# Kernel tuning notes

Hardware: AMD Instinct MI355X
Metric: run time of the kernel (lower is better)

The kernel has to match this reference:

```python
import jax, jax.numpy as jnp
import numpy as np

BLOCK_SIZE = 32
BLOCK_COUNTS = 4
NEG = -1e9
SEQ_LENS = np.array([512, 384, 448, 256], dtype=np.int64)


def setup_inputs():
    key = jax.random.key(0)
    ks = jax.random.split(key, 5)
    T = int(SEQ_LENS.sum()); H = 4; D = 64
    offs = np.concatenate([[0], np.cumsum(SEQ_LENS)]).astype(np.int64)
    return {
        "q": jax.random.normal(ks[0], (T, H, D), jnp.float32),
        "k": jax.random.normal(ks[1], (T, H, D), jnp.float32),
        "v": jax.random.normal(ks[2], (T, H, D), jnp.float32),
        "g_cmp": jax.random.uniform(ks[3], (T, H), jnp.float32),
        "g_slc": jax.random.uniform(ks[4], (T, H), jnp.float32),
        "x_offsets": jnp.asarray(offs),
    }


def _silu(x):
    return x * jax.nn.sigmoid(x)


def _forward(q, k, v, g_cmp, g_slc, offs):
    bs = BLOCK_SIZE
    B = len(offs) - 1
    seq_lens = offs[1:] - offs[:-1]              # np [B]
    T, H, D = q.shape
    max_n = int(seq_lens.max())
    nb = (max_n + bs - 1) // bs                  # max compressed blocks
    L = nb * bs                                  # padded length (multiple of bs)
    batch_ids = np.repeat(np.arange(B), seq_lens)
    local_ids = np.arange(T) - offs[:-1][batch_ids]

    def pad(x):  # jagged [T, ...] -> padded [B, L, ...]
        return jnp.zeros((B, L) + x.shape[1:], x.dtype).at[batch_ids, local_ids].set(x)

    pq, pk, pv = pad(q), pad(k), pad(v)
    # block-pooled (mean) compressed K/V; partial blocks also divided by bs, as in torch
    k_cmp = pk.reshape(B, nb, bs, H, D).sum(axis=2) / bs   # [B, nb, H, D]
    v_cmp = pv.reshape(B, nb, bs, H, D).sum(axis=2) / bs

    scale = D ** -0.5
    pos = np.arange(max_n)                       # local query positions
    qblk = pos // bs
    blk = np.arange(nb)
    causal = qblk[:, None] >= blk[None, :]       # [max_n, nb]
    seq_valid = pos[None, :] < seq_lens[:, None]  # [B, max_n]
    cmp_lens = (seq_lens + bs - 1) // bs
    blk_valid = blk[None, :] < cmp_lens[:, None]  # [B, nb]

    pq_m = pq[:, :max_n]                          # [B, max_n, H, D]
    scores = jnp.einsum('bqhd,bkhd->bhqk', pq_m, k_cmp) * scale  # [B,H,max_n,nb]

    # --- compressed branch: mask to -1e9, SiLU, zero masked (matches cmp kernel) ---
    m_full = (jnp.asarray(causal)[None, None]
              & jnp.asarray(seq_valid)[:, None, :, None]
              & jnp.asarray(blk_valid)[:, None, None, :])
    m_zero = jnp.asarray(causal)[None, None] & jnp.asarray(blk_valid)[:, None, None, :]
    p_cmp = jnp.where(m_zero, _silu(jnp.where(m_full, scores, NEG)), 0.0)
    o_cmp_pad = jnp.einsum('bhqk,bkhd->bqhd', p_cmp, v_cmp)
    o_cmp_pad = o_cmp_pad * pad(g_cmp)[:, :max_n, :, None]
    o_cmp = o_cmp_pad[batch_ids, local_ids]       # back to jagged [T,H,D]

    # --- per-token top-S block selection on causally masked compressed scores ---
    sel_scores = jnp.where(jnp.asarray(causal)[None, None], scores, -jnp.inf)
    S = min(BLOCK_COUNTS, nb)
    _, topk = jax.lax.top_k(sel_scores, S)        # [B,H,max_n,S] block ids

    # --- selected branch: gather raw K/V from the chosen blocks ---
    r = np.arange(bs)
    tpos = topk[..., None] * bs + r               # [B,H,max_n,S,bs] local key pos < L
    pk_h = pk.transpose(0, 2, 1, 3)               # [B,H,L,D]
    pv_h = pv.transpose(0, 2, 1, 3)
    idx = tpos.reshape(B, H, -1)
    k_sel = jnp.take_along_axis(pk_h, idx[..., None], axis=2).reshape(B, H, max_n, S, bs, D)
    v_sel = jnp.take_along_axis(pv_h, idx[..., None], axis=2).reshape(B, H, max_n, S, bs, D)
    pq_h = pq_m.transpose(0, 2, 1, 3)             # [B,H,max_n,D]
    s_slc = jnp.einsum('bhmd,bhmsrd->bhmsr', pq_h, k_sel) * scale
    within = tpos < jnp.asarray(seq_lens)[:, None, None, None, None]
    caus = tpos <= jnp.asarray(pos)[None, None, :, None, None]
    p_slc = jnp.where(within & caus, _silu(s_slc), 0.0)
    o_slc_pad = jnp.einsum('bhmsr,bhmsrd->bmhd', p_slc, v_sel)
    o_slc_pad = o_slc_pad * pad(g_slc)[:, :max_n, :, None]
    o_slc = o_slc_pad[batch_ids, local_ids]
    return o_cmp, o_slc


def reference(q, k, v, g_cmp, g_slc, x_offsets):
    return _forward(q, k, v, g_cmp, g_slc, np.asarray(x_offsets))
```

## Files before the change

kernel.cpp:

```cpp
#include <hip/hip_runtime.h>
#include <hip/hip_bf16.h>
#include <math.h>

#define HH 4
#define DD 64
#define BS 32
#define SSEL 4
#define STRIDE (HH * DD)

typedef __attribute__((ext_vector_type(8))) short bf16x8;
typedef __attribute__((ext_vector_type(4))) float f32x4;

__device__ __forceinline__ float silu_f(float x) { return x / (1.0f + __expf(-x)); }

__device__ __forceinline__ unsigned int pk2bf(float a, float b) {
    union { __hip_bfloat16 h[2]; unsigned int u; } cu;
    cu.h[0] = __float2bfloat16(a);
    cu.h[1] = __float2bfloat16(b);
    return cu.u;
}

__global__ __launch_bounds__(512, 2) void nsa_all(
        const float* __restrict__ q, const float* __restrict__ k,
        const float* __restrict__ v, const float* __restrict__ gc,
        const float* __restrict__ gs, const int* __restrict__ offs,
        int B, int T, float* __restrict__ out) {
    __shared__ float Qf[32][68];
    __shared__ float Kc[16][68];
    __shared__ float Vc[16][64];
    __shared__ unsigned int Msk[32];
    __shared__ unsigned short Qs[32][64];
    __shared__ __align__(16) char UN[4 * 32 * 68 * 4];

    unsigned int (*Pw)[32][20] = (unsigned int (*)[32][20])UN;
    float        (*Op)[32][68] = (float (*)[32][68])UN;

    int qbh = blockIdx.x;
    int h   = qbh & (HH - 1);
    int qb  = qbh / HH;

    int b = -1, lb = 0, cum = 0, off = 0, n = 0;
    for (int i = 0; i < B; ++i) {
        int o0 = offs[i], o1 = offs[i + 1];
        int nbi = (o1 - o0 + BS - 1) / BS;
        if (qb < cum + nbi) { b = i; lb = qb - cum; off = o0; n = o1 - o0; break; }
        cum += nbi;
    }
    if (b < 0) return;
    int t0  = off + lb * BS;
    int nbl = lb + 1;
    const float scale = 0.125f;
    int tid = threadIdx.x;
    int w = tid >> 6, lane = tid & 63;
    int l15 = lane & 15, g = lane >> 4;

    {
        int row = tid >> 4, dg = tid & 15;
        int trow = min(t0 + row, T - 1);
        float4 a = *(const float4*)(q + (size_t)trow * STRIDE + h * DD + dg * 4);
        a.x *= scale; a.y *= scale; a.z *= scale; a.w *= scale;
        *(float4*)&Qf[row][dg * 4] = a;
        uint2 uu = { pk2bf(a.x, a.y), pk2bf(a.z, a.w) };
        *(uint2*)&Qs[row][(((dg >> 1) ^ (row & 7)) * 8) + (dg & 1) * 4] = uu;
    }

    if (tid < nbl * 32) {
        int j = tid >> 5, rest = tid & 31, kind = rest >> 4, d4 = rest & 15;
        const float* base = (kind ? v : k) + (size_t)(off + j * BS) * STRIDE + h * DD + d4 * 4;
        float4 acc = {0.f, 0.f, 0.f, 0.f};
        #pragma unroll
        for (int r = 0; r < BS; ++r) {
            float4 x = *(const float4*)(base + (size_t)r * STRIDE);
            acc.x += x.x; acc.y += x.y; acc.z += x.z; acc.w += x.w;
        }
        acc.x *= (1.f / BS); acc.y *= (1.f / BS); acc.z *= (1.f / BS); acc.w *= (1.f / BS);
        if (kind) *(float4*)&Vc[j][d4 * 4] = acc;
        else      *(float4*)&Kc[j][d4 * 4] = acc;
    }
    __syncthreads();

    {
        int qq = tid >> 4, j = tid & 15;
        int base16 = lane & 48;
        float s = -INFINITY, p = 0.f;
        if (j < nbl) {
            s = 0.f;
            #pragma unroll
            for (int i = 0; i < 16; ++i) {
                float4 qv = *(float4*)&Qf[qq][i * 4];
                float4 kk = *(float4*)&Kc[j][i * 4];
                s += qv.x * kk.x + qv.y * kk.y + qv.z * kk.z + qv.w * kk.w;
            }
            p = silu_f(s);
        }
        int rank = 0;
        #pragma unroll
        for (int i = 0; i < 16; ++i) {
            float si = __shfl(s, base16 | i, 64);
            rank += (si > s) || (si == s && i < j);
        }
        bool sel = (j < nbl) && (rank < SSEL);
        unsigned long long bal = __ballot(sel);
        if (j == 0) Msk[qq] = (unsigned int)((bal >> base16) & 0xFFFFull);

        float4 o = {0.f, 0.f, 0.f, 0.f};
        for (int blk = 0; blk < nbl; ++blk) {
            float pb = __shfl(p, base16 | blk, 64);
            float4 vv = *(float4*)&Vc[blk][j * 4];
            o.x += pb * vv.x; o.y += pb * vv.y; o.z += pb * vv.z; o.w += pb * vv.w;
        }
        if (lb * BS + qq < n) {
            float gv = gc[(size_t)(t0 + qq) * HH + h];
            o.x *= gv; o.y *= gv; o.z *= gv; o.w *= gv;
            *(float4*)(out + (size_t)(t0 + qq) * STRIDE + h * DD + j * 4) = o;
        }
    }
    __syncthreads();

    unsigned int Msq[2];
    Msq[0] = Msk[l15];
    Msq[1] = Msk[16 + l15];

    f32x4 oacc[4][2];
    #pragma unroll
    for (int dt = 0; dt < 4; ++dt)
        #pragma unroll
        for (int qt = 0; qt < 2; ++qt)
            oacc[dt][qt] = (f32x4){0.f, 0.f, 0.f, 0.f};

    #pragma unroll 1
    for (int kb = w; kb <= lb; kb += 8) {
        const float* kbase = k + (size_t)(off + kb * BS) * STRIDE + h * DD;
        const float* vbase = v + (size_t)(off + kb * BS) * STRIDE + h * DD;

        float tv[4][8];
        #pragma unroll
        for (int dt = 0; dt < 4; ++dt)
            #pragma unroll
            for (int j = 0; j < 8; ++j)
                tv[dt][j] = vbase[(size_t)(g * 8 + j) * STRIDE + dt * 16 + l15];

        float4 kf[2][2][2];
        #pragma unroll
        for (int tt = 0; tt < 2; ++tt)
            #pragma unroll
            for (int ds = 0; ds < 2; ++ds) {
                const float4* p = (const float4*)(kbase + (size_t)(tt * 16 + l15) * STRIDE
                                                  + ds * 32 + g * 8);
                kf[tt][ds][0] = p[0];
                kf[tt][ds][1] = p[1];
            }

        bf16x8 a1[2][2];
        #pragma unroll
        for (int tt = 0; tt < 2; ++tt)
            #pragma unroll
            for (int ds = 0; ds < 2; ++ds) {
                union { unsigned int u[4]; bf16x8 v8; } cu;
                float4 x = kf[tt][ds][0], y = kf[tt][ds][1];
                cu.u[0] = pk2bf(x.x, x.y); cu.u[1] = pk2bf(x.z, x.w);
                cu.u[2] = pk2bf(y.x, y.y); cu.u[3] = pk2bf(y.z, y.w);
                a1[tt][ds] = cu.v8;
            }
        bf16x8 b1[2][2];
        #pragma unroll
        for (int ds = 0; ds < 2; ++ds)
            #pragma unroll
            for (int tt = 0; tt < 2; ++tt)
                b1[tt][ds] = *(bf16x8*)&Qs[tt * 16 + l15][((g + ds * 4) ^ (l15 & 7)) * 8];

        f32x4 s[2][2];
        #pragma unroll
        for (int kt = 0; kt < 2; ++kt)
            #pragma unroll
            for (int qt = 0; qt < 2; ++qt) {
                s[kt][qt] = (f32x4){0.f, 0.f, 0.f, 0.f};
                s[kt][qt] = __builtin_amdgcn_mfma_f32_16x16x32_bf16(a1[kt][0], b1[qt][0], s[kt][qt], 0, 0, 0);
                s[kt][qt] = __builtin_amdgcn_mfma_f32_16x16x32_bf16(a1[kt][1], b1[qt][1], s[kt][qt], 0, 0, 0);
            }

        #pragma unroll
        for (int kt = 0; kt < 2; ++kt)
            #pragma unroll
            for (int qt = 0; qt < 2; ++qt) {
                bool selbit = (Msq[qt] >> kb) & 1u;
                float pv[4];
                #pragma unroll
                for (int r = 0; r < 4; ++r) {
                    int k_l = kt * 16 + g * 4 + r;
                    int q_l = qt * 16 + l15;
                    bool ok = selbit && (kb < lb || k_l <= q_l);
                    pv[r] = ok ? silu_f(s[kt][qt][r]) : 0.f;
                }
                Pw[w][qt * 16 + l15][kt * 8 + g * 2 + 0] = pk2bf(pv[0], pv[1]);
                Pw[w][qt * 16 + l15][kt * 8 + g * 2 + 1] = pk2bf(pv[2], pv[3]);
            }
        bf16x8 b2[2];
        b2[0] = *(bf16x8*)&Pw[w][l15][g * 4];
        b2[1] = *(bf16x8*)&Pw[w][16 + l15][g * 4];

        bf16x8 a2[4];
        #pragma unroll
        for (int dt = 0; dt < 4; ++dt) {
            union { unsigned int u[4]; bf16x8 v8; } cu;
            cu.u[0] = pk2bf(tv[dt][0], tv[dt][1]);
            cu.u[1] = pk2bf(tv[dt][2], tv[dt][3]);
            cu.u[2] = pk2bf(tv[dt][4], tv[dt][5]);
            cu.u[3] = pk2bf(tv[dt][6], tv[dt][7]);
            a2[dt] = cu.v8;
        }

        #pragma unroll
        for (int dt = 0; dt < 4; ++dt)
            #pragma unroll
            for (int qt = 0; qt < 2; ++qt)
                oacc[dt][qt] = __builtin_amdgcn_mfma_f32_16x16x32_bf16(a2[dt], b2[qt], oacc[dt][qt], 0, 0, 0);
    }
    __syncthreads();

    if (w < 4) {
        #pragma unroll
        for (int dt = 0; dt < 4; ++dt)
            #pragma unroll
            for (int qt = 0; qt < 2; ++qt)
                #pragma unroll
                for (int r = 0; r < 4; ++r)
                    Op[w][qt * 16 + l15][dt * 16 + g * 4 + r] = oacc[dt][qt][r];
    }
    __syncthreads();
    if (w >= 4) {
        #pragma unroll
        for (int dt = 0; dt < 4; ++dt)
            #pragma unroll
            for (int qt = 0; qt < 2; ++qt)
                #pragma unroll
                for (int r = 0; r < 4; ++r)
                    Op[w - 4][qt * 16 + l15][dt * 16 + g * 4 + r] += oacc[dt][qt][r];
    }
    __syncthreads();

    {
        int qq = tid >> 4, dg = tid & 15;
        if (lb * BS + qq < n) {
            float gv = gs[(size_t)(t0 + qq) * HH + h];
            float o[4];
            #pragma unroll
            for (int i = 0; i < 4; ++i) {
                int d = dg * 4 + i;
                o[i] = (Op[0][qq][d] + Op[1][qq][d] + Op[2][qq][d] + Op[3][qq][d]) * gv;
            }
            *(float4*)(out + (size_t)T * STRIDE + (size_t)(t0 + qq) * STRIDE + h * DD + dg * 4)
                = (float4){o[0], o[1], o[2], o[3]};
        }
    }
}

extern "C" void kernel_launch(void* const* d_in, const int* in_sizes, int n_in,
                              void* d_out, int out_size, void* d_ws, size_t ws_size,
                              hipStream_t stream) {
    const float* q    = (const float*)d_in[0];
    const float* k    = (const float*)d_in[1];
    const float* v    = (const float*)d_in[2];
    const float* gc   = (const float*)d_in[3];
    const float* gs   = (const float*)d_in[4];
    const int*   offs = (const int*)d_in[5];

    int B = in_sizes[5] - 1;
    int T = out_size / (2 * STRIDE);
    int nbcap  = (T + BS - 1) / BS;
    int nqbcap = nbcap + B;

    nsa_all<<<dim3((unsigned)(nqbcap * HH)), dim3(512), 0, stream>>>(
        q, k, v, gc, gs, offs, B, T, (float*)d_out);
}
```

Measured before the change: 17.61 us.

## Hoist selected-branch K/V loads and QK MFMAs before compressed-branch work

Moves the per-warp loading of raw K/V blocks and the QK^T MFMA to the start of the kernel, before the compressed-branch pooling and top-k phase. This lets global-memory latency and MFMA work overlap with the compressed computation. Q fragments are now built straight from global memory into registers, which removes the swizzled Qs shared array. The loop is unrolled into at most two fixed iterations, so it assumes lb < 16 (sequences up to 512 tokens), and holding both iterations' data in registers raises register pressure.

```diff
diff --git a/kernel.cpp b/kernel.cpp
--- a/kernel.cpp
+++ b/kernel.cpp
@@ -29,7 +29,6 @@
     __shared__ float Kc[16][68];
     __shared__ float Vc[16][64];
     __shared__ unsigned int Msk[32];
-    __shared__ unsigned short Qs[32][64];
     __shared__ __align__(16) char UN[4 * 32 * 68 * 4];
 
     unsigned int (*Pw)[32][20] = (unsigned int (*)[32][20])UN;
@@ -54,14 +53,80 @@
     int w = tid >> 6, lane = tid & 63;
     int l15 = lane & 15, g = lane >> 4;
 
+    bool have0 = (w <= lb);
+    bool have1 = (w + 8 <= lb);
+
+    bf16x8 b1[2][2];
+    #pragma unroll
+    for (int qt = 0; qt < 2; ++qt)
+        #pragma unroll
+        for (int ds = 0; ds < 2; ++ds) {
+            int trow = min(t0 + qt * 16 + l15, T - 1);
+            const float4* p = (const float4*)(q + (size_t)trow * STRIDE + h * DD
+                                              + ds * 32 + g * 8);
+            float4 x = p[0], y = p[1];
+            union { unsigned int u[4]; bf16x8 v8; } cu;
+            cu.u[0] = pk2bf(x.x * scale, x.y * scale);
+            cu.u[1] = pk2bf(x.z * scale, x.w * scale);
+            cu.u[2] = pk2bf(y.x * scale, y.y * scale);
+            cu.u[3] = pk2bf(y.z * scale, y.w * scale);
+            b1[qt][ds] = cu.v8;
+        }
+
+#define LOAD_QKT(KB, A2, SS)                                                            \
+    {                                                                                   \
+        const float* kbase = k + (size_t)(off + (KB) * BS) * STRIDE + h * DD;           \
+        const float* vbase = v + (size_t)(off + (KB) * BS) * STRIDE + h * DD;           \
+        float tv[4][8];                                                                 \
+        _Pragma("unroll")                                                               \
+        for (int dt = 0; dt < 4; ++dt)                                                  \
+            _Pragma("unroll")                                                           \
+            for (int j = 0; j < 8; ++j)                                                 \
+                tv[dt][j] = vbase[(size_t)(g * 8 + j) * STRIDE + dt * 16 + l15];        \
+        bf16x8 a1[2][2];                                                                \
+        _Pragma("unroll")                                                               \
+        for (int tt = 0; tt < 2; ++tt)                                                  \
+            _Pragma("unroll")                                                           \
+            for (int ds = 0; ds < 2; ++ds) {                                            \
+                const float4* p = (const float4*)(kbase + (size_t)(tt * 16 + l15) * STRIDE \
+                                                  + ds * 32 + g * 8);                   \
+                float4 x = p[0], y = p[1];                                              \
+                union { unsigned int u[4]; bf16x8 v8; } cu;                             \
+                cu.u[0] = pk2bf(x.x, x.y); cu.u[1] = pk2bf(x.z, x.w);                   \
+                cu.u[2] = pk2bf(y.x, y.y); cu.u[3] = pk2bf(y.z, y.w);                   \
+                a1[tt][ds] = cu.v8;                                                     \
+            }                                                                           \
+        _Pragma("unroll")                                                               \
+        for (int dt = 0; dt < 4; ++dt) {                                                \
+            union { unsigned int u[4]; bf16x8 v8; } cu;                                 \
+            cu.u[0] = pk2bf(tv[dt][0], tv[dt][1]);                                      \
+            cu.u[1] = pk2bf(tv[dt][2], tv[dt][3]);                                      \
+            cu.u[2] = pk2bf(tv[dt][4], tv[dt][5]);                                      \
+            cu.u[3] = pk2bf(tv[dt][6], tv[dt][7]);                                      \
+            A2[dt] = cu.v8;                                                             \
+        }                                                                               \
+        _Pragma("unroll")                                                               \
+        for (int kt = 0; kt < 2; ++kt)                                                  \
+            _Pragma("unroll")                                                           \
+            for (int qt = 0; qt < 2; ++qt) {                                            \
+                SS[kt][qt] = (f32x4){0.f, 0.f, 0.f, 0.f};                               \
+                SS[kt][qt] = __builtin_amdgcn_mfma_f32_16x16x32_bf16(a1[kt][0], b1[qt][0], SS[kt][qt], 0, 0, 0); \
+                SS[kt][qt] = __builtin_amdgcn_mfma_f32_16x16x32_bf16(a1[kt][1], b1[qt][1], SS[kt][qt], 0, 0, 0); \
+            }                                                                           \
+    }
+
+    bf16x8 a2A[4], a2B[4];
+    f32x4  sA[2][2], sB[2][2];
+    if (have0) LOAD_QKT(w, a2A, sA)
+    if (have1) LOAD_QKT(w + 8, a2B, sB)
+#undef LOAD_QKT
+
     {
         int row = tid >> 4, dg = tid & 15;
         int trow = min(t0 + row, T - 1);
         float4 a = *(const float4*)(q + (size_t)trow * STRIDE + h * DD + dg * 4);
         a.x *= scale; a.y *= scale; a.z *= scale; a.w *= scale;
         *(float4*)&Qf[row][dg * 4] = a;
-        uint2 uu = { pk2bf(a.x, a.y), pk2bf(a.z, a.w) };
-        *(uint2*)&Qs[row][(((dg >> 1) ^ (row & 7)) * 8) + (dg & 1) * 4] = uu;
     }
 
     if (tid < nbl * 32) {
@@ -128,94 +193,38 @@
         for (int qt = 0; qt < 2; ++qt)
             oacc[dt][qt] = (f32x4){0.f, 0.f, 0.f, 0.f};
 
-    #pragma unroll 1
-    for (int kb = w; kb <= lb; kb += 8) {
-        const float* kbase = k + (size_t)(off + kb * BS) * STRIDE + h * DD;
-        const float* vbase = v + (size_t)(off + kb * BS) * STRIDE + h * DD;
-
-        float tv[4][8];
-        #pragma unroll
-        for (int dt = 0; dt < 4; ++dt)
-            #pragma unroll
-            for (int j = 0; j < 8; ++j)
-                tv[dt][j] = vbase[(size_t)(g * 8 + j) * STRIDE + dt * 16 + l15];
-
-        float4 kf[2][2][2];
-        #pragma unroll
-        for (int tt = 0; tt < 2; ++tt)
-            #pragma unroll
-            for (int ds = 0; ds < 2; ++ds) {
-                const float4* p = (const float4*)(kbase + (size_t)(tt * 16 + l15) * STRIDE
-                                                  + ds * 32 + g * 8);
-                kf[tt][ds][0] = p[0];
-                kf[tt][ds][1] = p[1];
-            }
-
-        bf16x8 a1[2][2];
-        #pragma unroll
-        for (int tt = 0; tt < 2; ++tt)
-            #pragma unroll
-            for (int ds = 0; ds < 2; ++ds) {
-                union { unsigned int u[4]; bf16x8 v8; } cu;
-                float4 x = kf[tt][ds][0], y = kf[tt][ds][1];
-                cu.u[0] = pk2bf(x.x, x.y); cu.u[1] = pk2bf(x.z, x.w);
-                cu.u[2] = pk2bf(y.x, y.y); cu.u[3] = pk2bf(y.z, y.w);
-                a1[tt][ds] = cu.v8;
-            }
-        bf16x8 b1[2][2];
-        #pragma unroll
-        for (int ds = 0; ds < 2; ++ds)
-            #pragma unroll
-            for (int tt = 0; tt < 2; ++tt)
-                b1[tt][ds] = *(bf16x8*)&Qs[tt * 16 + l15][((g + ds * 4) ^ (l15 & 7)) * 8];
-
-        f32x4 s[2][2];
-        #pragma unroll
-        for (int kt = 0; kt < 2; ++kt)
-            #pragma unroll
-            for (int qt = 0; qt < 2; ++qt) {
-                s[kt][qt] = (f32x4){0.f, 0.f, 0.f, 0.f};
-                s[kt][qt] = __builtin_amdgcn_mfma_f32_16x16x32_bf16(a1[kt][0], b1[qt][0], s[kt][qt], 0, 0, 0);
-                s[kt][qt] = __builtin_amdgcn_mfma_f32_16x16x32_bf16(a1[kt][1], b1[qt][1], s[kt][qt], 0, 0, 0);
-            }
-
-        #pragma unroll
-        for (int kt = 0; kt < 2; ++kt)
-            #pragma unroll
-            for (int qt = 0; qt < 2; ++qt) {
-                bool selbit = (Msq[qt] >> kb) & 1u;
-                float pv[4];
-                #pragma unroll
-                for (int r = 0; r < 4; ++r) {
-                    int k_l = kt * 16 + g * 4 + r;
-                    int q_l = qt * 16 + l15;
-                    bool ok = selbit && (kb < lb || k_l <= q_l);
-                    pv[r] = ok ? silu_f(s[kt][qt][r]) : 0.f;
-                }
-                Pw[w][qt * 16 + l15][kt * 8 + g * 2 + 0] = pk2bf(pv[0], pv[1]);
-                Pw[w][qt * 16 + l15][kt * 8 + g * 2 + 1] = pk2bf(pv[2], pv[3]);
-            }
-        bf16x8 b2[2];
-        b2[0] = *(bf16x8*)&Pw[w][l15][g * 4];
-        b2[1] = *(bf16x8*)&Pw[w][16 + l15][g * 4];
-
-        bf16x8 a2[4];
-        #pragma unroll
-        for (int dt = 0; dt < 4; ++dt) {
-            union { unsigned int u[4]; bf16x8 v8; } cu;
-            cu.u[0] = pk2bf(tv[dt][0], tv[dt][1]);
-            cu.u[1] = pk2bf(tv[dt][2], tv[dt][3]);
-            cu.u[2] = pk2bf(tv[dt][4], tv[dt][5]);
-            cu.u[3] = pk2bf(tv[dt][6], tv[dt][7]);
-            a2[dt] = cu.v8;
-        }
-
-        #pragma unroll
-        for (int dt = 0; dt < 4; ++dt)
-            #pragma unroll
-            for (int qt = 0; qt < 2; ++qt)
-                oacc[dt][qt] = __builtin_amdgcn_mfma_f32_16x16x32_bf16(a2[dt], b2[qt], oacc[dt][qt], 0, 0, 0);
-    }
+#define FINISH(KB, A2, SS)                                                              \
+    {                                                                                   \
+        const int kb = (KB);                                                            \
+        _Pragma("unroll")                                                               \
+        for (int kt = 0; kt < 2; ++kt)                                                  \
+            _Pragma("unroll")                                                           \
+            for (int qt = 0; qt < 2; ++qt) {                                            \
+                bool selbit = (Msq[qt] >> kb) & 1u;                                     \
+                float pv[4];                                                            \
+                _Pragma("unroll")                                                       \
+                for (int r = 0; r < 4; ++r) {                                           \
+                    int k_l = kt * 16 + g * 4 + r;                                      \
+                    int q_l = qt * 16 + l15;                                            \
+                    bool ok = selbit && (kb < lb || k_l <= q_l);                        \
+                    pv[r] = ok ? silu_f(SS[kt][qt][r]) : 0.f;                           \
+                }                                                                       \
+                Pw[w][qt * 16 + l15][kt * 8 + g * 2 + 0] = pk2bf(pv[0], pv[1]);         \
+                Pw[w][qt * 16 + l15][kt * 8 + g * 2 + 1] = pk2bf(pv[2], pv[3]);         \
+            }                                                                           \
+        bf16x8 b2[2];                                                                   \
+        b2[0] = *(bf16x8*)&Pw[w][l15][g * 4];                                           \
+        b2[1] = *(bf16x8*)&Pw[w][16 + l15][g * 4];                                      \
+        _Pragma("unroll")                                                               \
+        for (int dt = 0; dt < 4; ++dt)                                                  \
+            _Pragma("unroll")                                                           \
+            for (int qt = 0; qt < 2; ++qt)                                              \
+                oacc[dt][qt] = __builtin_amdgcn_mfma_f32_16x16x32_bf16(A2[dt], b2[qt], oacc[dt][qt], 0, 0, 0); \
+    }
+
+    if (have0) FINISH(w, a2A, sA)
+    if (have1) FINISH(w + 8, a2B, sB)
+#undef FINISH
     __syncthreads();
 
     if (w < 4) {
```

Measured after the change: 20.40 us. +15.9%, slower.

## Double block to 1024 threads: one key block per wave, split pooling

Applied to the files above, without the earlier changes.

Workgroups grow from 512 to 1024 threads (16 waves), so each wave handles exactly one key block instead of looping over blocks with stride 8. Compressed K/V pooling is split across two half-blocks per thread with a shared-memory partial reduction. The cross-wave output reduction now sums eight partial planes, which doubles the shared-memory scratch area. The risks are lower occupancy, since launch bounds drop to one block per CU target, plus an extra barrier and more LDS traffic in the final reduction.

```diff
diff --git a/kernel.cpp b/kernel.cpp
--- a/kernel.cpp
+++ b/kernel.cpp
@@ -20,7 +20,7 @@
     return cu.u;
 }
 
-__global__ __launch_bounds__(512, 2) void nsa_all(
+__global__ __launch_bounds__(1024, 1) void nsa_all(
         const float* __restrict__ q, const float* __restrict__ k,
         const float* __restrict__ v, const float* __restrict__ gc,
         const float* __restrict__ gs, const int* __restrict__ offs,
@@ -30,10 +30,11 @@
     __shared__ float Vc[16][64];
     __shared__ unsigned int Msk[32];
     __shared__ unsigned short Qs[32][64];
-    __shared__ __align__(16) char UN[4 * 32 * 68 * 4];
-
-    unsigned int (*Pw)[32][20] = (unsigned int (*)[32][20])UN;
-    float        (*Op)[32][68] = (float (*)[32][68])UN;
+    __shared__ __align__(16) char UN[8 * 32 * 68 * 4];
+
+    float4       (*Pt)[2][2][16] = (float4 (*)[2][2][16])UN;
+    unsigned int (*Pw)[32][20]   = (unsigned int (*)[32][20])UN;
+    float        (*Op)[32][68]   = (float (*)[32][68])UN;
 
     int qbh = blockIdx.x;
     int h   = qbh & (HH - 1);
@@ -54,7 +55,21 @@
     int w = tid >> 6, lane = tid & 63;
     int l15 = lane & 15, g = lane >> 4;
 
-    {
+    if (tid < nbl * 64) {
+        int j = tid >> 6, rest = tid & 63;
+        int kind = rest >> 5, rh = (rest >> 4) & 1, d4 = rest & 15;
+        const float* base = (kind ? v : k)
+            + (size_t)(off + j * BS + rh * 16) * STRIDE + h * DD + d4 * 4;
+        float4 acc = {0.f, 0.f, 0.f, 0.f};
+        #pragma unroll
+        for (int r = 0; r < 16; ++r) {
+            float4 x = *(const float4*)(base + (size_t)r * STRIDE);
+            acc.x += x.x; acc.y += x.y; acc.z += x.z; acc.w += x.w;
+        }
+        Pt[j][kind][rh][d4] = acc;
+    }
+
+    if (tid < 512) {
         int row = tid >> 4, dg = tid & 15;
         int trow = min(t0 + row, T - 1);
         float4 a = *(const float4*)(q + (size_t)trow * STRIDE + h * DD + dg * 4);
@@ -63,23 +78,20 @@
         uint2 uu = { pk2bf(a.x, a.y), pk2bf(a.z, a.w) };
         *(uint2*)&Qs[row][(((dg >> 1) ^ (row & 7)) * 8) + (dg & 1) * 4] = uu;
     }
+    __syncthreads();
 
     if (tid < nbl * 32) {
         int j = tid >> 5, rest = tid & 31, kind = rest >> 4, d4 = rest & 15;
-        const float* base = (kind ? v : k) + (size_t)(off + j * BS) * STRIDE + h * DD + d4 * 4;
-        float4 acc = {0.f, 0.f, 0.f, 0.f};
-        #pragma unroll
-        for (int r = 0; r < BS; ++r) {
-            float4 x = *(const float4*)(base + (size_t)r * STRIDE);
-            acc.x += x.x; acc.y += x.y; acc.z += x.z; acc.w += x.w;
-        }
-        acc.x *= (1.f / BS); acc.y *= (1.f / BS); acc.z *= (1.f / BS); acc.w *= (1.f / BS);
-        if (kind) *(float4*)&Vc[j][d4 * 4] = acc;
-        else      *(float4*)&Kc[j][d4 * 4] = acc;
-    }
-    __syncthreads();
-
-    {
+        float4 a = Pt[j][kind][0][d4], c = Pt[j][kind][1][d4];
+        float4 r;
+        r.x = (a.x + c.x) * (1.f / BS); r.y = (a.y + c.y) * (1.f / BS);
+        r.z = (a.z + c.z) * (1.f / BS); r.w = (a.w + c.w) * (1.f / BS);
+        if (kind) *(float4*)&Vc[j][d4 * 4] = r;
+        else      *(float4*)&Kc[j][d4 * 4] = r;
+    }
+    __syncthreads();
+
+    if (tid < 512) {
         int qq = tid >> 4, j = tid & 15;
         int base16 = lane & 48;
         float s = -INFINITY, p = 0.f;
@@ -117,10 +129,6 @@
     }
     __syncthreads();
 
-    unsigned int Msq[2];
-    Msq[0] = Msk[l15];
-    Msq[1] = Msk[16 + l15];
-
     f32x4 oacc[4][2];
     #pragma unroll
     for (int dt = 0; dt < 4; ++dt)
@@ -128,8 +136,12 @@
         for (int qt = 0; qt < 2; ++qt)
             oacc[dt][qt] = (f32x4){0.f, 0.f, 0.f, 0.f};
 
-    #pragma unroll 1
-    for (int kb = w; kb <= lb; kb += 8) {
+    if (w <= lb) {
+        const int kb = w;
+        unsigned int Msq[2];
+        Msq[0] = Msk[l15];
+        Msq[1] = Msk[16 + l15];
+
         const float* kbase = k + (size_t)(off + kb * BS) * STRIDE + h * DD;
         const float* vbase = v + (size_t)(off + kb * BS) * STRIDE + h * DD;
 
@@ -218,7 +230,7 @@
     }
     __syncthreads();
 
-    if (w < 4) {
+    if (w < 8) {
         #pragma unroll
         for (int dt = 0; dt < 4; ++dt)
             #pragma unroll
@@ -228,18 +240,18 @@
                     Op[w][qt * 16 + l15][dt * 16 + g * 4 + r] = oacc[dt][qt][r];
     }
     __syncthreads();
-    if (w >= 4) {
+    if (w >= 8) {
         #pragma unroll
         for (int dt = 0; dt < 4; ++dt)
             #pragma unroll
             for (int qt = 0; qt < 2; ++qt)
                 #pragma unroll
                 for (int r = 0; r < 4; ++r)
-                    Op[w - 4][qt * 16 + l15][dt * 16 + g * 4 + r] += oacc[dt][qt][r];
-    }
-    __syncthreads();
-
-    {
+                    Op[w - 8][qt * 16 + l15][dt * 16 + g * 4 + r] += oacc[dt][qt][r];
+    }
+    __syncthreads();
+
+    if (tid < 512) {
         int qq = tid >> 4, dg = tid & 15;
         if (lb * BS + qq < n) {
             float gv = gs[(size_t)(t0 + qq) * HH + h];
@@ -247,7 +259,10 @@
             #pragma unroll
             for (int i = 0; i < 4; ++i) {
                 int d = dg * 4 + i;
-                o[i] = (Op[0][qq][d] + Op[1][qq][d] + Op[2][qq][d] + Op[3][qq][d]) * gv;
+                float acc = 0.f;
+                #pragma unroll
+                for (int pl = 0; pl < 8; ++pl) acc += Op[pl][qq][d];
+                o[i] = acc * gv;
             }
             *(float4*)(out + (size_t)T * STRIDE + (size_t)(t0 + qq) * STRIDE + h * DD + dg * 4)
                 = (float4){o[0], o[1], o[2], o[3]};
@@ -270,6 +285,6 @@
     int nbcap  = (T + BS - 1) / BS;
     int nqbcap = nbcap + B;
 
-    nsa_all<<<dim3((unsigned)(nqbcap * HH)), dim3(512), 0, stream>>>(
+    nsa_all<<<dim3((unsigned)(nqbcap * HH)), dim3(1024), 0, stream>>>(
         q, k, v, gc, gs, offs, B, T, (float*)d_out);
 }
```

Measured after the change: 18.38 us. 1.04x slower.

## Hoist first selected-block QK^T before compressed phase and add MFMA priority hints

Applied to the files above, without the earlier changes.

Peels the first iteration of the per-warp selected-block loop and moves its K/V global loads, Q loading (read directly from global and converted to bf16) and QK^T MFMAs to the start of the kernel, before the compressed-branch work and barriers. This lets that memory latency overlap with the compressed-attention phase. The loop is replaced by at most two explicit blocks, relying on lb < 16, and s_setprio is raised around MFMA sections. The cost is higher register pressure from keeping sA and a2A live across the compressed phase, plus duplicated Q reads.

```diff
diff --git a/kernel.cpp b/kernel.cpp
--- a/kernel.cpp
+++ b/kernel.cpp
@@ -54,6 +54,80 @@
     int w = tid >> 6, lane = tid & 63;
     int l15 = lane & 15, g = lane >> 4;
 
+    bool have0 = (w <= lb);
+    bool have1 = (w + 8 <= lb);
+
+    bf16x8 a2A[4];
+    f32x4  sA[2][2];
+    if (have0) {
+        const float* kbase = k + (size_t)(off + w * BS) * STRIDE + h * DD;
+        const float* vbase = v + (size_t)(off + w * BS) * STRIDE + h * DD;
+
+        float tv[4][8];
+        #pragma unroll
+        for (int dt = 0; dt < 4; ++dt)
+            #pragma unroll
+            for (int j = 0; j < 8; ++j)
+                tv[dt][j] = vbase[(size_t)(g * 8 + j) * STRIDE + dt * 16 + l15];
+
+        float4 kf[2][2][2];
+        #pragma unroll
+        for (int tt = 0; tt < 2; ++tt)
+            #pragma unroll
+            for (int ds = 0; ds < 2; ++ds) {
+                const float4* p = (const float4*)(kbase + (size_t)(tt * 16 + l15) * STRIDE
+                                                  + ds * 32 + g * 8);
+                kf[tt][ds][0] = p[0];
+                kf[tt][ds][1] = p[1];
+            }
+
+        bf16x8 b1e[2][2];
+        #pragma unroll
+        for (int qt = 0; qt < 2; ++qt)
+            #pragma unroll
+            for (int ds = 0; ds < 2; ++ds) {
+                int trow = min(t0 + qt * 16 + l15, T - 1);
+                const float4* p = (const float4*)(q + (size_t)trow * STRIDE + h * DD
+                                                  + ds * 32 + g * 8);
+                float4 x = p[0], y = p[1];
+                union { unsigned int u[4]; bf16x8 v8; } cu;
+                cu.u[0] = pk2bf(x.x * scale, x.y * scale);
+                cu.u[1] = pk2bf(x.z * scale, x.w * scale);
+                cu.u[2] = pk2bf(y.x * scale, y.y * scale);
+                cu.u[3] = pk2bf(y.z * scale, y.w * scale);
+                b1e[qt][ds] = cu.v8;
+            }
+
+        bf16x8 a1[2][2];
+        #pragma unroll
+        for (int tt = 0; tt < 2; ++tt)
+            #pragma unroll
+            for (int ds = 0; ds < 2; ++ds) {
+                union { unsigned int u[4]; bf16x8 v8; } cu;
+                float4 x = kf[tt][ds][0], y = kf[tt][ds][1];
+                cu.u[0] = pk2bf(x.x, x.y); cu.u[1] = pk2bf(x.z, x.w);
+                cu.u[2] = pk2bf(y.x, y.y); cu.u[3] = pk2bf(y.z, y.w);
+                a1[tt][ds] = cu.v8;
+            }
+        #pragma unroll
+        for (int dt = 0; dt < 4; ++dt) {
+            union { unsigned int u[4]; bf16x8 v8; } cu;
+            cu.u[0] = pk2bf(tv[dt][0], tv[dt][1]);
+            cu.u[1] = pk2bf(tv[dt][2], tv[dt][3]);
+            cu.u[2] = pk2bf(tv[dt][4], tv[dt][5]);
+            cu.u[3] = pk2bf(tv[dt][6], tv[dt][7]);
+            a2A[dt] = cu.v8;
+        }
+        #pragma unroll
+        for (int kt = 0; kt < 2; ++kt)
+            #pragma unroll
+            for (int qt = 0; qt < 2; ++qt) {
+                sA[kt][qt] = (f32x4){0.f, 0.f, 0.f, 0.f};
+                sA[kt][qt] = __builtin_amdgcn_mfma_f32_16x16x32_bf16(a1[kt][0], b1e[qt][0], sA[kt][qt], 0, 0, 0);
+                sA[kt][qt] = __builtin_amdgcn_mfma_f32_16x16x32_bf16(a1[kt][1], b1e[qt][1], sA[kt][qt], 0, 0, 0);
+            }
+    }
+
     {
         int row = tid >> 4, dg = tid & 15;
         int trow = min(t0 + row, T - 1);
@@ -128,10 +202,43 @@
         for (int qt = 0; qt < 2; ++qt)
             oacc[dt][qt] = (f32x4){0.f, 0.f, 0.f, 0.f};
 
-    #pragma unroll 1
-    for (int kb = w; kb <= lb; kb += 8) {
-        const float* kbase = k + (size_t)(off + kb * BS) * STRIDE + h * DD;
-        const float* vbase = v + (size_t)(off + kb * BS) * STRIDE + h * DD;
+#define FINISH(KB, A2, SS)                                                              \
+    {                                                                                   \
+        const int kb = (KB);                                                            \
+        _Pragma("unroll")                                                               \
+        for (int kt = 0; kt < 2; ++kt)                                                  \
+            _Pragma("unroll")                                                           \
+            for (int qt = 0; qt < 2; ++qt) {                                            \
+                bool selbit = (Msq[qt] >> kb) & 1u;                                     \
+                float pv[4];                                                            \
+                _Pragma("unroll")                                                       \
+                for (int r = 0; r < 4; ++r) {                                           \
+                    int k_l = kt * 16 + g * 4 + r;                                      \
+                    int q_l = qt * 16 + l15;                                            \
+                    bool ok = selbit && (kb < lb || k_l <= q_l);                        \
+                    pv[r] = ok ? silu_f(SS[kt][qt][r]) : 0.f;                           \
+                }                                                                       \
+                Pw[w][qt * 16 + l15][kt * 8 + g * 2 + 0] = pk2bf(pv[0], pv[1]);         \
+                Pw[w][qt * 16 + l15][kt * 8 + g * 2 + 1] = pk2bf(pv[2], pv[3]);         \
+            }                                                                           \
+        bf16x8 b2[2];                                                                   \
+        b2[0] = *(bf16x8*)&Pw[w][l15][g * 4];                                           \
+        b2[1] = *(bf16x8*)&Pw[w][16 + l15][g * 4];                                      \
+        __builtin_amdgcn_s_setprio(1);                                                  \
+        _Pragma("unroll")                                                               \
+        for (int dt = 0; dt < 4; ++dt)                                                  \
+            _Pragma("unroll")                                                           \
+            for (int qt = 0; qt < 2; ++qt)                                              \
+                oacc[dt][qt] = __builtin_amdgcn_mfma_f32_16x16x32_bf16(A2[dt], b2[qt], oacc[dt][qt], 0, 0, 0); \
+        __builtin_amdgcn_s_setprio(0);                                                  \
+    }
+
+    if (have0) FINISH(w, a2A, sA)
+
+    if (have1) {
+        const int kb1 = w + 8;
+        const float* kbase = k + (size_t)(off + kb1 * BS) * STRIDE + h * DD;
+        const float* vbase = v + (size_t)(off + kb1 * BS) * STRIDE + h * DD;
 
         float tv[4][8];
         #pragma unroll
@@ -169,37 +276,7 @@
             for (int tt = 0; tt < 2; ++tt)
                 b1[tt][ds] = *(bf16x8*)&Qs[tt * 16 + l15][((g + ds * 4) ^ (l15 & 7)) * 8];
 
-        f32x4 s[2][2];
-        #pragma unroll
-        for (int kt = 0; kt < 2; ++kt)
-            #pragma unroll
-            for (int qt = 0; qt < 2; ++qt) {
-                s[kt][qt] = (f32x4){0.f, 0.f, 0.f, 0.f};
-                s[kt][qt] = __builtin_amdgcn_mfma_f32_16x16x32_bf16(a1[kt][0], b1[qt][0], s[kt][qt], 0, 0, 0);
-                s[kt][qt] = __builtin_amdgcn_mfma_f32_16x16x32_bf16(a1[kt][1], b1[qt][1], s[kt][qt], 0, 0, 0);
-            }
-
-        #pragma unroll
-        for (int kt = 0; kt < 2; ++kt)
-            #pragma unroll
-            for (int qt = 0; qt < 2; ++qt) {
-                bool selbit = (Msq[qt] >> kb) & 1u;
-                float pv[4];
-                #pragma unroll
-                for (int r = 0; r < 4; ++r) {
-                    int k_l = kt * 16 + g * 4 + r;
-                    int q_l = qt * 16 + l15;
-                    bool ok = selbit && (kb < lb || k_l <= q_l);
-                    pv[r] = ok ? silu_f(s[kt][qt][r]) : 0.f;
-                }
-                Pw[w][qt * 16 + l15][kt * 8 + g * 2 + 0] = pk2bf(pv[0], pv[1]);
-                Pw[w][qt * 16 + l15][kt * 8 + g * 2 + 1] = pk2bf(pv[2], pv[3]);
-            }
-        bf16x8 b2[2];
-        b2[0] = *(bf16x8*)&Pw[w][l15][g * 4];
-        b2[1] = *(bf16x8*)&Pw[w][16 + l15][g * 4];
-
-        bf16x8 a2[4];
+        bf16x8 a2B[4];
         #pragma unroll
         for (int dt = 0; dt < 4; ++dt) {
             union { unsigned int u[4]; bf16x8 v8; } cu;
@@ -207,15 +284,24 @@
             cu.u[1] = pk2bf(tv[dt][2], tv[dt][3]);
             cu.u[2] = pk2bf(tv[dt][4], tv[dt][5]);
             cu.u[3] = pk2bf(tv[dt][6], tv[dt][7]);
-            a2[dt] = cu.v8;
-        }
-
-        #pragma unroll
-        for (int dt = 0; dt < 4; ++dt)
-            #pragma unroll
-            for (int qt = 0; qt < 2; ++qt)
-                oacc[dt][qt] = __builtin_amdgcn_mfma_f32_16x16x32_bf16(a2[dt], b2[qt], oacc[dt][qt], 0, 0, 0);
-    }
+            a2B[dt] = cu.v8;
+        }
+
+        f32x4 sB[2][2];
+        __builtin_amdgcn_s_setprio(1);
+        #pragma unroll
+        for (int kt = 0; kt < 2; ++kt)
+            #pragma unroll
+            for (int qt = 0; qt < 2; ++qt) {
+                sB[kt][qt] = (f32x4){0.f, 0.f, 0.f, 0.f};
+                sB[kt][qt] = __builtin_amdgcn_mfma_f32_16x16x32_bf16(a1[kt][0], b1[qt][0], sB[kt][qt], 0, 0, 0);
+                sB[kt][qt] = __builtin_amdgcn_mfma_f32_16x16x32_bf16(a1[kt][1], b1[qt][1], sB[kt][qt], 0, 0, 0);
+            }
+        __builtin_amdgcn_s_setprio(0);
+
+        FINISH(kb1, a2B, sB)
+    }
+#undef FINISH
     __syncthreads();
 
     if (w < 4) {
```

After: 20.25 us. 1.15x slower.
